# Performance work log

Hardware: AMD Instinct MI355X
Metric: run time of the kernel (lower is better)

The kernel has to match this reference:

```python
import jax, jax.numpy as jnp
import numpy as np

B, T, F, H, D, L = 64, 1024, 304, 304, 128, 128  # batch, enc len, feat=emb, hidden, dict_size, max_phn_num


def _init(k, sh):
    bound = 1.0 / np.sqrt(H)
    return jax.random.uniform(k, sh, jnp.float32, -bound, bound)


def setup_inputs() -> dict:
    key = jax.random.key(0)
    ks = jax.random.split(key, 12)
    return {
        "x": jax.random.normal(ks[0], (B, T, F), jnp.float32),
        "target": jax.random.randint(ks[1], (B, L, 1), 0, D),
        "emb": jax.random.normal(ks[2], (D, F), jnp.float32),
        "enc_Wih": _init(ks[3], (3 * H, F)),
        "enc_Whh": _init(ks[4], (3 * H, H)),
        "enc_bih": _init(ks[5], (3 * H,)),
        "enc_bhh": _init(ks[6], (3 * H,)),
        "dec_Wih": _init(ks[7], (3 * H, F)),
        "dec_Whh": _init(ks[8], (3 * H, H)),
        "dec_bih": _init(ks[9], (3 * H,)),
        "dec_bhh": _init(ks[10], (3 * H,)),
        "lin_W": _init(ks[11], (D, H)),
        "lin_b": jnp.zeros((D,), jnp.float32),
    }


def gru_step(h, xt, Wih, Whh, bih, bhh):
    # PyTorch GRU cell, gate order (r, z, n)
    gi = xt @ Wih.T + bih            # [B, 3H]
    gh = h @ Whh.T + bhh             # [B, 3H]
    ir, iz, innew = jnp.split(gi, 3, axis=-1)
    hr, hz, hn = jnp.split(gh, 3, axis=-1)
    r = jax.nn.sigmoid(ir + hr)
    z = jax.nn.sigmoid(iz + hz)
    n = jnp.tanh(innew + r * hn)
    return (1.0 - z) * n + z * h


def reference(x, target, emb, enc_Wih, enc_Whh, enc_bih, enc_bhh,
              dec_Wih, dec_Whh, dec_bih, dec_bhh, lin_W, lin_b):
    Bsz = x.shape[0]
    Hdim = enc_Whh.shape[1]
    Lphn = target.shape[1]

    # ---- encoder GRU over acoustic frames ----
    h0 = jnp.zeros((Bsz, Hdim), x.dtype)

    def enc_scan(h, xt):
        return gru_step(h, xt, enc_Wih, enc_Whh, enc_bih, enc_bhh), None

    h_enc, _ = jax.lax.scan(enc_scan, h0, jnp.swapaxes(x, 0, 1))

    tok0 = target[:, 0, 0]  # [B]

    def dec_scan(carry, _):
        h, tok = carry
        e = emb[tok]                                   # [B, F]
        h = gru_step(h, e, dec_Wih, dec_Whh, dec_bih, dec_bhh)
        logits = h @ lin_W.T + lin_b                   # [B, D]
        nxt = jnp.argmax(logits, axis=-1)
        return (h, nxt), logits

    _, logits = jax.lax.scan(dec_scan, (h_enc, tok0), None, length=Lphn)
    softmaxs = jnp.swapaxes(logits, 0, 1)              # [B, L, D]

    softmax_cal = softmaxs[:, :-1, :].reshape(-1, softmaxs.shape[-1])
    target_cal = target[:, 1:, :].reshape(-1)
    asr_outputs = jnp.argmax(softmaxs[:, :-1, :], axis=2)[:, :, None]
    return softmax_cal, target_cal, asr_outputs
```

## Files before the change

kernel.cpp:

```cpp
#include <hip/hip_runtime.h>
#include <cstdint>
#include <cstddef>

#define HN 304
#define G3 912
#define US 76
#define RS 228
#define NB 64
#define TSTEPS 1024
#define LDEC 127
#define DCLS 128

#define OUT_O1 1040384
#define OUT_O2 1048512

static const size_t OFF_GI   = 0;
static const size_t OFF_HP   = 239075328ull;
static const size_t OFF_AM   = 239230976ull;
static const size_t OFF_ABRT = 239233024ull;
static const size_t OFF_TAB  = 239233280ull;
static const size_t WS_NEED  = 239700224ull;

__global__ __launch_bounds__(256) void gi_gemm(const float* __restrict__ X,
                                               const float* __restrict__ W,
                                               const float* __restrict__ bias,
                                               float* __restrict__ out)
{
    __shared__ float As[16][132];
    __shared__ float Bs[16][132];
    const int tid = threadIdx.x;
    const int m0 = blockIdx.x * 128;
    const int n0 = blockIdx.y * 128;
    const int tx = tid & 15;
    const int ty = tid >> 4;
    const int lr = tid >> 1;
    const int lc = (tid & 1) * 8;

    float c[8][8];
#pragma unroll
    for (int i = 0; i < 8; ++i)
#pragma unroll
        for (int j = 0; j < 8; ++j) c[i][j] = 0.f;

    const bool wok = (n0 + lr < G3);
    const float* xrow = X + (size_t)(m0 + lr) * HN;
    const float* wrow = W + (size_t)(n0 + lr) * HN;
    const float4 z4 = make_float4(0.f, 0.f, 0.f, 0.f);

    float4 xa = *(const float4*)(xrow + lc);
    float4 xb = *(const float4*)(xrow + lc + 4);
    float4 wa = wok ? *(const float4*)(wrow + lc) : z4;
    float4 wb = wok ? *(const float4*)(wrow + lc + 4) : z4;

    for (int k0 = 0; k0 < HN; k0 += 16) {
        As[lc + 0][lr] = xa.x; As[lc + 1][lr] = xa.y; As[lc + 2][lr] = xa.z; As[lc + 3][lr] = xa.w;
        As[lc + 4][lr] = xb.x; As[lc + 5][lr] = xb.y; As[lc + 6][lr] = xb.z; As[lc + 7][lr] = xb.w;
        Bs[lc + 0][lr] = wa.x; Bs[lc + 1][lr] = wa.y; Bs[lc + 2][lr] = wa.z; Bs[lc + 3][lr] = wa.w;
        Bs[lc + 4][lr] = wb.x; Bs[lc + 5][lr] = wb.y; Bs[lc + 6][lr] = wb.z; Bs[lc + 7][lr] = wb.w;
        __syncthreads();
        if (k0 + 16 < HN) {
            xa = *(const float4*)(xrow + k0 + 16 + lc);
            xb = *(const float4*)(xrow + k0 + 16 + lc + 4);
            if (wok) {
                wa = *(const float4*)(wrow + k0 + 16 + lc);
                wb = *(const float4*)(wrow + k0 + 16 + lc + 4);
            }
        }
#pragma unroll
        for (int kk = 0; kk < 16; ++kk) {
            const float4 a0 = *(const float4*)&As[kk][ty * 8];
            const float4 a1 = *(const float4*)&As[kk][ty * 8 + 4];
            const float4 b0 = *(const float4*)&Bs[kk][tx * 8];
            const float4 b1 = *(const float4*)&Bs[kk][tx * 8 + 4];
            c[0][0] += a0.x * b0.x; c[0][1] += a0.x * b0.y; c[0][2] += a0.x * b0.z; c[0][3] += a0.x * b0.w;
            c[0][4] += a0.x * b1.x; c[0][5] += a0.x * b1.y; c[0][6] += a0.x * b1.z; c[0][7] += a0.x * b1.w;
            c[1][0] += a0.y * b0.x; c[1][1] += a0.y * b0.y; c[1][2] += a0.y * b0.z; c[1][3] += a0.y * b0.w;
            c[1][4] += a0.y * b1.x; c[1][5] += a0.y * b1.y; c[1][6] += a0.y * b1.z; c[1][7] += a0.y * b1.w;
            c[2][0] += a0.z * b0.x; c[2][1] += a0.z * b0.y; c[2][2] += a0.z * b0.z; c[2][3] += a0.z * b0.w;
            c[2][4] += a0.z * b1.x; c[2][5] += a0.z * b1.y; c[2][6] += a0.z * b1.z; c[2][7] += a0.z * b1.w;
            c[3][0] += a0.w * b0.x; c[3][1] += a0.w * b0.y; c[3][2] += a0.w * b0.z; c[3][3] += a0.w * b0.w;
            c[3][4] += a0.w * b1.x; c[3][5] += a0.w * b1.y; c[3][6] += a0.w * b1.z; c[3][7] += a0.w * b1.w;
            c[4][0] += a1.x * b0.x; c[4][1] += a1.x * b0.y; c[4][2] += a1.x * b0.z; c[4][3] += a1.x * b0.w;
            c[4][4] += a1.x * b1.x; c[4][5] += a1.x * b1.y; c[4][6] += a1.x * b1.z; c[4][7] += a1.x * b1.w;
            c[5][0] += a1.y * b0.x; c[5][1] += a1.y * b0.y; c[5][2] += a1.y * b0.z; c[5][3] += a1.y * b0.w;
            c[5][4] += a1.y * b1.x; c[5][5] += a1.y * b1.y; c[5][6] += a1.y * b1.z; c[5][7] += a1.y * b1.w;
            c[6][0] += a1.z * b0.x; c[6][1] += a1.z * b0.y; c[6][2] += a1.z * b0.z; c[6][3] += a1.z * b0.w;
            c[6][4] += a1.z * b1.x; c[6][5] += a1.z * b1.y; c[6][6] += a1.z * b1.z; c[6][7] += a1.z * b1.w;
            c[7][0] += a1.w * b0.x; c[7][1] += a1.w * b0.y; c[7][2] += a1.w * b0.z; c[7][3] += a1.w * b0.w;
            c[7][4] += a1.w * b1.x; c[7][5] += a1.w * b1.y; c[7][6] += a1.w * b1.z; c[7][7] += a1.w * b1.w;
        }
        __syncthreads();
    }

    const int nb = n0 + tx * 8;
    float4 bb0 = (nb + 3 < G3) ? *(const float4*)(bias + nb) : z4;
    float4 bb1 = (nb + 7 < G3) ? *(const float4*)(bias + nb + 4) : z4;
#pragma unroll
    for (int i = 0; i < 8; ++i) {
        const size_t m = (size_t)(m0 + ty * 8 + i);
        if (nb + 3 < G3) {
            float4 v = make_float4(c[i][0] + bb0.x, c[i][1] + bb0.y, c[i][2] + bb0.z, c[i][3] + bb0.w);
            *(float4*)(out + m * G3 + nb) = v;
        }
        if (nb + 7 < G3) {
            float4 v = make_float4(c[i][4] + bb1.x, c[i][5] + bb1.y, c[i][6] + bb1.z, c[i][7] + bb1.w);
            *(float4*)(out + m * G3 + nb + 4) = v;
        }
    }
}

__global__ __launch_bounds__(256) void table_k(const float* __restrict__ emb,
                                               const float* __restrict__ Wih,
                                               const float* __restrict__ bih,
                                               float* __restrict__ tab)
{
    const int idx = blockIdx.x * 256 + threadIdx.x;
    const int d = idx / G3;
    const int R = idx - d * G3;
    const float4* e4 = (const float4*)(emb + (size_t)d * HN);
    const float4* w4 = (const float4*)(Wih + (size_t)R * HN);
    float acc = 0.f;
#pragma unroll
    for (int j = 0; j < 76; ++j) {
        const float4 e = e4[j], w = w4[j];
        acc += e.x * w.x; acc += e.y * w.y; acc += e.z * w.z; acc += e.w * w.w;
    }
    tab[idx] = acc + bih[R];
}

__global__ void tcal_k(const int* __restrict__ target, float* __restrict__ out)
{
    const int i = blockIdx.x * 256 + threadIdx.x;
    if (i < NB * LDEC) {
        const int b = i / LDEC;
        const int t = i - b * LDEC;
        out[OUT_O1 + i] = (float)target[b * 128 + t + 1];
    }
}

__device__ __forceinline__ unsigned poll_tag32(unsigned int* p, unsigned want, int* abortf)
{
    unsigned v; int g = 0;
    for (;;) {
        v = __hip_atomic_load(p, __ATOMIC_RELAXED, __HIP_MEMORY_SCOPE_AGENT);
        if ((v & 3u) == want) break;
        if ((++g & 255) == 0) {
            if (__hip_atomic_load(abortf, __ATOMIC_RELAXED, __HIP_MEMORY_SCOPE_AGENT) != 0) break;
            if (g > (1 << 19)) {
                __hip_atomic_store(abortf, 1, __ATOMIC_RELAXED, __HIP_MEMORY_SCOPE_AGENT);
                break;
            }
        }
    }
    __asm__ volatile("" ::: "memory");
    return v;
}

__device__ __forceinline__ unsigned long long spin_tag(unsigned long long* p, int want, int* abortf)
{
    int g = 0;
    unsigned long long r;
    for (;;) {
        r = __hip_atomic_load(p, __ATOMIC_RELAXED, __HIP_MEMORY_SCOPE_AGENT);
        if ((int)(r >> 32) >= want) break;
        if ((++g & 255) == 0) {
            if (__hip_atomic_load(abortf, __ATOMIC_RELAXED, __HIP_MEMORY_SCOPE_AGENT) != 0) break;
            if (g > (1 << 19)) {
                __hip_atomic_store(abortf, 1, __ATOMIC_RELAXED, __HIP_MEMORY_SCOPE_AGENT);
                break;
            }
        }
    }
    __asm__ volatile("" ::: "memory");
    return r;
}

__global__ __launch_bounds__(512, 2) void rnn_persist(
    const float* __restrict__ gi,
    const float* __restrict__ encWhh, const float* __restrict__ encBhh,
    const float* __restrict__ decWhh, const float* __restrict__ decBhh,
    const float* __restrict__ tab,
    const float* __restrict__ linW, const float* __restrict__ linB,
    const int* __restrict__ target,
    unsigned int* hpk, unsigned long long* amax, int* abortf, float* out)
{
    const int w = blockIdx.x;
    const int b = w & 63;
    const int s = w >> 6;
    const int tid = threadIdx.x;

    __shared__ alignas(16) float hbuf[HN];
    __shared__ alignas(16) float part[4][RS];
    __shared__ alignas(16) float lpart[32][9];
    __shared__ float logit_s[32];
    __shared__ float amx_v[4];
    __shared__ int   amx_i[4];

    const bool comp = (tid < 456);
    const int ksq = tid / 114;
    const int lp  = tid - ksq * 114;
    const int g0 = lp / US,        ul0 = lp - g0 * US;
    const int g1 = (lp + 114) / US, ul1 = (lp + 114) - g1 * US;
    const int Rrow0 = g0 * HN + s * US + ul0;
    const int Rrow1 = g1 * HN + s * US + ul1;
    const int u = s * US + tid;
    const int cq = tid / US;

    unsigned long long* amx = amax + b * 4;
    unsigned int* hpb = hpk + b * HN;

    float4 wreg0[19], wreg1[19];
    if (comp) {
        const float4* wp0 = (const float4*)(encWhh + (size_t)Rrow0 * HN + (size_t)ksq * US);
        const float4* wp1 = (const float4*)(encWhh + (size_t)Rrow1 * HN + (size_t)ksq * US);
#pragma unroll
        for (int j = 0; j < 19; ++j) { wreg0[j] = wp0[j]; wreg1[j] = wp1[j]; }
    }
    float b_r = 0.f, b_z = 0.f, b_n = 0.f;
    if (tid < US) { b_r = encBhh[u]; b_z = encBhh[HN + u]; b_n = encBhh[2 * HN + u]; }

    for (int i = tid; i < HN; i += 512) hbuf[i] = 0.f;
    __syncthreads();

    const float* gib = gi + (size_t)b * TSTEPS * G3;

    for (int t = 0; t < TSTEPS; ++t) {
        const int T = t + 1;
        float gr = 0.f, gz = 0.f, gn = 0.f;
        if (tid < US) {
            const float* gp = gib + (size_t)t * G3;
            gr = gp[u]; gz = gp[HN + u]; gn = gp[2 * HN + u];
        }
        if (comp) {
            const float4* hp = (const float4*)(hbuf + ksq * US);
            float acc0 = 0.f, acc1 = 0.f;
#pragma unroll
            for (int j = 0; j < 19; ++j) {
                const float4 h4 = hp[j];
                const float4 w0 = wreg0[j], w1 = wreg1[j];
                acc0 += w0.x * h4.x; acc0 += w0.y * h4.y; acc0 += w0.z * h4.z; acc0 += w0.w * h4.w;
                acc1 += w1.x * h4.x; acc1 += w1.y * h4.y; acc1 += w1.z * h4.z; acc1 += w1.w * h4.w;
            }
            part[ksq][lp] = acc0;
            part[ksq][lp + 114] = acc1;
        }
        __syncthreads();
        if (tid < US) {
            const float ghr = part[0][tid] + part[1][tid] + part[2][tid] + part[3][tid] + b_r;
            const float ghz = part[0][US + tid] + part[1][US + tid] + part[2][US + tid] + part[3][US + tid] + b_z;
            const float ghn = part[0][2 * US + tid] + part[1][2 * US + tid] + part[2][2 * US + tid] + part[3][2 * US + tid] + b_n;
            const float r = 1.f / (1.f + expf(-(gr + ghr)));
            const float z = 1.f / (1.f + expf(-(gz + ghz)));
            const float n = tanhf(gn + r * ghn);
            const float hnew = (1.f - z) * n + z * hbuf[u];
            const unsigned hb = (__float_as_uint(hnew) & ~3u) | ((unsigned)T & 3u);
            hbuf[u] = __uint_as_float(hb);
            __hip_atomic_store(&hpb[(T & 1) * NB * HN + u], hb,
                               __ATOMIC_RELAXED, __HIP_MEMORY_SCOPE_AGENT);
        }
        if (tid < HN && cq != s) {
            const unsigned v = poll_tag32(&hpb[(T & 1) * NB * HN + tid],
                                          (unsigned)T & 3u, abortf);
            hbuf[tid] = __uint_as_float(v);
        }
        __syncthreads();
    }

    if (comp) {
        const float4* wp0 = (const float4*)(decWhh + (size_t)Rrow0 * HN + (size_t)ksq * US);
        const float4* wp1 = (const float4*)(decWhh + (size_t)Rrow1 * HN + (size_t)ksq * US);
#pragma unroll
        for (int j = 0; j < 19; ++j) { wreg0[j] = wp0[j]; wreg1[j] = wp1[j]; }
    }
    if (tid < US) { b_r = decBhh[u]; b_z = decBhh[HN + u]; b_n = decBhh[2 * HN + u]; }
    int tok = target[b * 128];
    const int lrow = tid >> 3;
    const int lks = tid & 7;
    __syncthreads();

    for (int t = 0; t < LDEC; ++t) {
        const int T = TSTEPS + 1 + t;
        float gr = 0.f, gz = 0.f, gn = 0.f;
        if (tid < US) {
            const float* tp = tab + (size_t)tok * G3;
            gr = tp[u]; gz = tp[HN + u]; gn = tp[2 * HN + u];
        }
        if (comp) {
            const float4* hp = (const float4*)(hbuf + ksq * US);
            float acc0 = 0.f, acc1 = 0.f;
#pragma unroll
            for (int j = 0; j < 19; ++j) {
                const float4 h4 = hp[j];
                const float4 w0 = wreg0[j], w1 = wreg1[j];
                acc0 += w0.x * h4.x; acc0 += w0.y * h4.y; acc0 += w0.z * h4.z; acc0 += w0.w * h4.w;
                acc1 += w1.x * h4.x; acc1 += w1.y * h4.y; acc1 += w1.z * h4.z; acc1 += w1.w * h4.w;
            }
            part[ksq][lp] = acc0;
            part[ksq][lp + 114] = acc1;
        }
        __syncthreads();
        if (tid < US) {
            const float ghr = part[0][tid] + part[1][tid] + part[2][tid] + part[3][tid] + b_r;
            const float ghz = part[0][US + tid] + part[1][US + tid] + part[2][US + tid] + part[3][US + tid] + b_z;
            const float ghn = part[0][2 * US + tid] + part[1][2 * US + tid] + part[2][2 * US + tid] + part[3][2 * US + tid] + b_n;
            const float r = 1.f / (1.f + expf(-(gr + ghr)));
            const float z = 1.f / (1.f + expf(-(gz + ghz)));
            const float n = tanhf(gn + r * ghn);
            const float hnew = (1.f - z) * n + z * hbuf[u];
            const unsigned hb = (__float_as_uint(hnew) & ~3u) | ((unsigned)T & 3u);
            hbuf[u] = __uint_as_float(hb);
            __hip_atomic_store(&hpb[(T & 1) * NB * HN + u], hb,
                               __ATOMIC_RELAXED, __HIP_MEMORY_SCOPE_AGENT);
        }
        if (tid < HN && cq != s) {
            const unsigned v = poll_tag32(&hpb[(T & 1) * NB * HN + tid],
                                          (unsigned)T & 3u, abortf);
            hbuf[tid] = __uint_as_float(v);
        }
        __syncthreads();

        if (tid < 256) {
            const float2* wl = (const float2*)(linW + (size_t)(s * 32 + lrow) * HN + (size_t)lks * 38);
            const float2* hl = (const float2*)(hbuf + lks * 38);
            float a = 0.f;
#pragma unroll
            for (int j = 0; j < 19; ++j) { const float2 wv = wl[j], hv = hl[j]; a += wv.x * hv.x; a += wv.y * hv.y; }
            lpart[lrow][lks] = a;
        }
        __syncthreads();
        if (tid < 32) {
            const float lg = lpart[tid][0] + lpart[tid][1] + lpart[tid][2] + lpart[tid][3]
                           + lpart[tid][4] + lpart[tid][5] + lpart[tid][6] + lpart[tid][7]
                           + linB[s * 32 + tid];
            logit_s[tid] = lg;
            out[((size_t)b * LDEC + t) * DCLS + s * 32 + tid] = lg;
        }
        __syncthreads();
        if (tid == 0) {
            float bv = logit_s[0]; int bi = 0;
            for (int i = 1; i < 32; ++i) { const float v = logit_s[i]; if (v > bv) { bv = v; bi = i; } }
            const unsigned tagf = (unsigned)(((t + 1) << 8) | (s * 32 + bi));
            const unsigned long long pk = ((unsigned long long)tagf << 32) | (unsigned long long)__float_as_uint(bv);
            __hip_atomic_store(&amx[s], pk, __ATOMIC_RELAXED, __HIP_MEMORY_SCOPE_AGENT);
        }
        if (tid < 4) {
            const unsigned long long r = spin_tag(&amx[tid], (t + 1) << 8, abortf);
            amx_v[tid] = __uint_as_float((unsigned)r);
            amx_i[tid] = (int)(r >> 32) & 255;
        }
        __syncthreads();
        {
            float gbv = amx_v[0]; int gbi = amx_i[0];
            if (amx_v[1] > gbv) { gbv = amx_v[1]; gbi = amx_i[1]; }
            if (amx_v[2] > gbv) { gbv = amx_v[2]; gbi = amx_i[2]; }
            if (amx_v[3] > gbv) { gbv = amx_v[3]; gbi = amx_i[3]; }
            tok = gbi;
            if (tid == 0 && s == 0) out[OUT_O2 + (size_t)b * LDEC + t] = (float)gbi;
        }
    }
}

extern "C" void kernel_launch(void* const* d_in, const int* in_sizes, int n_in,
                              void* d_out, int out_size, void* d_ws, size_t ws_size,
                              hipStream_t stream)
{
    (void)in_sizes; (void)n_in; (void)out_size;
    const float* x      = (const float*)d_in[0];
    const int*   target = (const int*)  d_in[1];
    const float* emb    = (const float*)d_in[2];
    const float* encWih = (const float*)d_in[3];
    const float* encWhh = (const float*)d_in[4];
    const float* encBih = (const float*)d_in[5];
    const float* encBhh = (const float*)d_in[6];
    const float* decWih = (const float*)d_in[7];
    const float* decWhh = (const float*)d_in[8];
    const float* decBih = (const float*)d_in[9];
    const float* decBhh = (const float*)d_in[10];
    const float* linW   = (const float*)d_in[11];
    const float* linB   = (const float*)d_in[12];
    float* out = (float*)d_out;
    char* ws = (char*)d_ws;

    if (ws_size < WS_NEED) return;

    float*              gi   = (float*)(ws + OFF_GI);
    unsigned int*       hpk  = (unsigned int*)(ws + OFF_HP);
    unsigned long long* amax = (unsigned long long*)(ws + OFF_AM);
    int*                abrt = (int*)(ws + OFF_ABRT);
    float*              tab  = (float*)(ws + OFF_TAB);

    hipMemsetAsync(ws + OFF_HP, 0, OFF_TAB - OFF_HP, stream);
    gi_gemm<<<dim3(512, 8), 256, 0, stream>>>(x, encWih, encBih, gi);
    table_k<<<456, 256, 0, stream>>>(emb, decWih, decBih, tab);
    tcal_k<<<32, 256, 0, stream>>>(target, out);
    rnn_persist<<<256, 512, 0, stream>>>(gi, encWhh, encBhh, decWhh, decBhh, tab,
                                         linW, linB, target, hpk, amax, abrt, out);
}
```

Before: 3.064 ms.

## Compute full logits redundantly per block to drop cross-block argmax exchange

Each of the four blocks per batch row now stages all of lin_W in shared memory, computes all 128 logits itself and takes a local argmax, which removes the per-step global atomic publish/spin on the amax slots. The encoder loop is also unrolled by two so the next step's gate inputs are loaded ahead, and __syncthreads is replaced by a lighter lgkmcnt+s_barrier. The cost is about 160KB of dynamic shared memory per block, which may limit residency, plus four times the logit work.

Result: slower. 3.179 ms (+3.8%).

```diff
diff --git a/kernel.cpp b/kernel.cpp
--- a/kernel.cpp
+++ b/kernel.cpp
@@ -20,6 +20,14 @@
 static const size_t OFF_ABRT = 239233024ull;
 static const size_t OFF_TAB  = 239233280ull;
 static const size_t WS_NEED  = 239700224ull;
+
+#define SM_LINW   0
+#define SM_U      39040
+#define SM_HB     40192
+#define SM_AMXV   40496
+#define SM_AMXI   40500
+#define SM_FLOATS 40512
+#define SMEM_BYTES (SM_FLOATS * 4)
 
 __global__ __launch_bounds__(256) void gi_gemm(const float* __restrict__ X,
                                                const float* __restrict__ W,
@@ -138,6 +146,16 @@
     }
 }
 
+__device__ __forceinline__ void barl()
+{
+    asm volatile("s_waitcnt lgkmcnt(0)\n\ts_barrier" ::: "memory");
+}
+
+__device__ __forceinline__ void pub32(unsigned int* p, unsigned v)
+{
+    __hip_atomic_store(p, v, __ATOMIC_RELAXED, __HIP_MEMORY_SCOPE_AGENT);
+}
+
 __device__ __forceinline__ unsigned poll_tag32(unsigned int* p, unsigned want, int* abortf)
 {
     unsigned v; int g = 0;
@@ -156,24 +174,45 @@
     return v;
 }
 
-__device__ __forceinline__ unsigned long long spin_tag(unsigned long long* p, int want, int* abortf)
-{
-    int g = 0;
-    unsigned long long r;
-    for (;;) {
-        r = __hip_atomic_load(p, __ATOMIC_RELAXED, __HIP_MEMORY_SCOPE_AGENT);
-        if ((int)(r >> 32) >= want) break;
-        if ((++g & 255) == 0) {
-            if (__hip_atomic_load(abortf, __ATOMIC_RELAXED, __HIP_MEMORY_SCOPE_AGENT) != 0) break;
-            if (g > (1 << 19)) {
-                __hip_atomic_store(abortf, 1, __ATOMIC_RELAXED, __HIP_MEMORY_SCOPE_AGENT);
-                break;
-            }
-        }
-    }
-    __asm__ volatile("" ::: "memory");
-    return r;
-}
+#define RNN_STEP(T_, GR, GZ, GN) do {                                               \
+    if (comp) {                                                                     \
+        const float4* hp = (const float4*)(hbuf + ksq * US);                        \
+        float acc0 = 0.f, acc1 = 0.f;                                               \
+        _Pragma("unroll")                                                           \
+        for (int j = 0; j < 19; ++j) {                                              \
+            const float4 h4 = hp[j];                                                \
+            const float4 w0 = wreg0[j], w1 = wreg1[j];                              \
+            acc0 += w0.x * h4.x; acc0 += w0.y * h4.y;                               \
+            acc0 += w0.z * h4.z; acc0 += w0.w * h4.w;                               \
+            acc1 += w1.x * h4.x; acc1 += w1.y * h4.y;                               \
+            acc1 += w1.z * h4.z; acc1 += w1.w * h4.w;                               \
+        }                                                                           \
+        partU[ksq * RS + lp] = acc0;                                                \
+        partU[ksq * RS + lp + 114] = acc1;                                          \
+    }                                                                               \
+    barl();                                                                         \
+    if (tid < US) {                                                                 \
+        const float ghr = partU[tid] + partU[RS + tid]                              \
+                        + partU[2 * RS + tid] + partU[3 * RS + tid] + b_r;          \
+        const float ghz = partU[US + tid] + partU[RS + US + tid]                    \
+                        + partU[2 * RS + US + tid] + partU[3 * RS + US + tid] + b_z;\
+        const float ghn = partU[2 * US + tid] + partU[RS + 2 * US + tid]            \
+                        + partU[2 * RS + 2 * US + tid] + partU[3 * RS + 2 * US + tid] + b_n; \
+        const float r_ = 1.f / (1.f + expf(-((GR) + ghr)));                         \
+        const float z_ = 1.f / (1.f + expf(-((GZ) + ghz)));                         \
+        const float n_ = tanhf((GN) + r_ * ghn);                                    \
+        const float hnew = (1.f - z_) * n_ + z_ * hbuf[u];                          \
+        const unsigned hb_ = (__float_as_uint(hnew) & ~3u) | ((unsigned)(T_) & 3u); \
+        hbuf[u] = __uint_as_float(hb_);                                             \
+        pub32(&hpb[((T_) & 1) * NB * HN + u], hb_);                                 \
+    }                                                                               \
+    if (tid < HN && cq != s) {                                                      \
+        const unsigned v_ = poll_tag32(&hpb[((T_) & 1) * NB * HN + tid],            \
+                                       (unsigned)(T_) & 3u, abortf);                \
+        hbuf[tid] = __uint_as_float(v_);                                            \
+    }                                                                               \
+    barl();                                                                         \
+} while (0)
 
 __global__ __launch_bounds__(512, 2) void rnn_persist(
     const float* __restrict__ gi,
@@ -182,32 +221,37 @@
     const float* __restrict__ tab,
     const float* __restrict__ linW, const float* __restrict__ linB,
     const int* __restrict__ target,
-    unsigned int* hpk, unsigned long long* amax, int* abortf, float* out)
+    unsigned int* hpk, int* abortf, float* out)
 {
     const int w = blockIdx.x;
     const int b = w & 63;
     const int s = w >> 6;
     const int tid = threadIdx.x;
 
-    __shared__ alignas(16) float hbuf[HN];
-    __shared__ alignas(16) float part[4][RS];
-    __shared__ alignas(16) float lpart[32][9];
-    __shared__ float logit_s[32];
-    __shared__ float amx_v[4];
-    __shared__ int   amx_i[4];
+    extern __shared__ float smem[];
+    float* linw_s = smem + SM_LINW;
+    float* partU  = smem + SM_U;
+    float* hbuf   = smem + SM_HB;
+    float* amx_vs = smem + SM_AMXV;
+    int*   amx_is = (int*)(smem + SM_AMXI);
 
     const bool comp = (tid < 456);
     const int ksq = tid / 114;
     const int lp  = tid - ksq * 114;
-    const int g0 = lp / US,        ul0 = lp - g0 * US;
+    const int g0 = lp / US,         ul0 = lp - g0 * US;
     const int g1 = (lp + 114) / US, ul1 = (lp + 114) - g1 * US;
     const int Rrow0 = g0 * HN + s * US + ul0;
     const int Rrow1 = g1 * HN + s * US + ul1;
     const int u = s * US + tid;
     const int cq = tid / US;
 
-    unsigned long long* amx = amax + b * 4;
     unsigned int* hpb = hpk + b * HN;
+
+    for (int i = tid; i < DCLS * HN; i += 512) {
+        const int r0 = i / HN;
+        linw_s[r0 * 305 + (i - r0 * HN)] = linW[i];
+    }
+    for (int i = tid; i < HN; i += 512) hbuf[i] = 0.f;
 
     float4 wreg0[19], wreg1[19];
     if (comp) {
@@ -219,51 +263,24 @@
     float b_r = 0.f, b_z = 0.f, b_n = 0.f;
     if (tid < US) { b_r = encBhh[u]; b_z = encBhh[HN + u]; b_n = encBhh[2 * HN + u]; }
 
-    for (int i = tid; i < HN; i += 512) hbuf[i] = 0.f;
     __syncthreads();
 
     const float* gib = gi + (size_t)b * TSTEPS * G3;
 
-    for (int t = 0; t < TSTEPS; ++t) {
-        const int T = t + 1;
-        float gr = 0.f, gz = 0.f, gn = 0.f;
+    float grA = 0.f, gzA = 0.f, gnA = 0.f, grB = 0.f, gzB = 0.f, gnB = 0.f;
+    if (tid < US) { grA = gib[u]; gzA = gib[HN + u]; gnA = gib[2 * HN + u]; }
+
+    for (int t = 0; t < TSTEPS; t += 2) {
         if (tid < US) {
-            const float* gp = gib + (size_t)t * G3;
-            gr = gp[u]; gz = gp[HN + u]; gn = gp[2 * HN + u];
-        }
-        if (comp) {
-            const float4* hp = (const float4*)(hbuf + ksq * US);
-            float acc0 = 0.f, acc1 = 0.f;
-#pragma unroll
-            for (int j = 0; j < 19; ++j) {
-                const float4 h4 = hp[j];
-                const float4 w0 = wreg0[j], w1 = wreg1[j];
-                acc0 += w0.x * h4.x; acc0 += w0.y * h4.y; acc0 += w0.z * h4.z; acc0 += w0.w * h4.w;
-                acc1 += w1.x * h4.x; acc1 += w1.y * h4.y; acc1 += w1.z * h4.z; acc1 += w1.w * h4.w;
-            }
-            part[ksq][lp] = acc0;
-            part[ksq][lp + 114] = acc1;
-        }
-        __syncthreads();
-        if (tid < US) {
-            const float ghr = part[0][tid] + part[1][tid] + part[2][tid] + part[3][tid] + b_r;
-            const float ghz = part[0][US + tid] + part[1][US + tid] + part[2][US + tid] + part[3][US + tid] + b_z;
-            const float ghn = part[0][2 * US + tid] + part[1][2 * US + tid] + part[2][2 * US + tid] + part[3][2 * US + tid] + b_n;
-            const float r = 1.f / (1.f + expf(-(gr + ghr)));
-            const float z = 1.f / (1.f + expf(-(gz + ghz)));
-            const float n = tanhf(gn + r * ghn);
-            const float hnew = (1.f - z) * n + z * hbuf[u];
-            const unsigned hb = (__float_as_uint(hnew) & ~3u) | ((unsigned)T & 3u);
-            hbuf[u] = __uint_as_float(hb);
-            __hip_atomic_store(&hpb[(T & 1) * NB * HN + u], hb,
-                               __ATOMIC_RELAXED, __HIP_MEMORY_SCOPE_AGENT);
-        }
-        if (tid < HN && cq != s) {
-            const unsigned v = poll_tag32(&hpb[(T & 1) * NB * HN + tid],
-                                          (unsigned)T & 3u, abortf);
-            hbuf[tid] = __uint_as_float(v);
-        }
-        __syncthreads();
+            const float* gp = gib + (size_t)(t + 1) * G3;
+            grB = gp[u]; gzB = gp[HN + u]; gnB = gp[2 * HN + u];
+        }
+        RNN_STEP(t + 1, grA, gzA, gnA);
+        if (tid < US && t + 2 < TSTEPS) {
+            const float* gp = gib + (size_t)(t + 2) * G3;
+            grA = gp[u]; gzA = gp[HN + u]; gnA = gp[2 * HN + u];
+        }
+        RNN_STEP(t + 2, grB, gzB, gnB);
     }
 
     if (comp) {
@@ -274,9 +291,11 @@
     }
     if (tid < US) { b_r = decBhh[u]; b_z = decBhh[HN + u]; b_n = decBhh[2 * HN + u]; }
     int tok = target[b * 128];
-    const int lrow = tid >> 3;
-    const int lks = tid & 7;
-    __syncthreads();
+    float linb_r = 0.f;
+    if (tid < DCLS) linb_r = linB[tid];
+    const int lr128 = tid & 127;
+    const int lq = tid >> 7;
+    barl();
 
     for (int t = 0; t < LDEC; ++t) {
         const int T = TSTEPS + 1 + t;
@@ -285,75 +304,50 @@
             const float* tp = tab + (size_t)tok * G3;
             gr = tp[u]; gz = tp[HN + u]; gn = tp[2 * HN + u];
         }
-        if (comp) {
-            const float4* hp = (const float4*)(hbuf + ksq * US);
-            float acc0 = 0.f, acc1 = 0.f;
+        RNN_STEP(T, gr, gz, gn);
+
+        {
+            const float* wl = linw_s + lr128 * 305 + lq * 76;
+            const float* hl = hbuf + lq * 76;
+            float a0 = 0.f, a1 = 0.f;
 #pragma unroll
             for (int j = 0; j < 19; ++j) {
-                const float4 h4 = hp[j];
-                const float4 w0 = wreg0[j], w1 = wreg1[j];
-                acc0 += w0.x * h4.x; acc0 += w0.y * h4.y; acc0 += w0.z * h4.z; acc0 += w0.w * h4.w;
-                acc1 += w1.x * h4.x; acc1 += w1.y * h4.y; acc1 += w1.z * h4.z; acc1 += w1.w * h4.w;
-            }
-            part[ksq][lp] = acc0;
-            part[ksq][lp + 114] = acc1;
-        }
-        __syncthreads();
-        if (tid < US) {
-            const float ghr = part[0][tid] + part[1][tid] + part[2][tid] + part[3][tid] + b_r;
-            const float ghz = part[0][US + tid] + part[1][US + tid] + part[2][US + tid] + part[3][US + tid] + b_z;
-            const float ghn = part[0][2 * US + tid] + part[1][2 * US + tid] + part[2][2 * US + tid] + part[3][2 * US + tid] + b_n;
-            const float r = 1.f / (1.f + expf(-(gr + ghr)));
-            const float z = 1.f / (1.f + expf(-(gz + ghz)));
-            const float n = tanhf(gn + r * ghn);
-            const float hnew = (1.f - z) * n + z * hbuf[u];
-            const unsigned hb = (__float_as_uint(hnew) & ~3u) | ((unsigned)T & 3u);
-            hbuf[u] = __uint_as_float(hb);
-            __hip_atomic_store(&hpb[(T & 1) * NB * HN + u], hb,
-                               __ATOMIC_RELAXED, __HIP_MEMORY_SCOPE_AGENT);
-        }
-        if (tid < HN && cq != s) {
-            const unsigned v = poll_tag32(&hpb[(T & 1) * NB * HN + tid],
-                                          (unsigned)T & 3u, abortf);
-            hbuf[tid] = __uint_as_float(v);
-        }
-        __syncthreads();
-
-        if (tid < 256) {
-            const float2* wl = (const float2*)(linW + (size_t)(s * 32 + lrow) * HN + (size_t)lks * 38);
-            const float2* hl = (const float2*)(hbuf + lks * 38);
-            float a = 0.f;
-#pragma unroll
-            for (int j = 0; j < 19; ++j) { const float2 wv = wl[j], hv = hl[j]; a += wv.x * hv.x; a += wv.y * hv.y; }
-            lpart[lrow][lks] = a;
-        }
-        __syncthreads();
-        if (tid < 32) {
-            const float lg = lpart[tid][0] + lpart[tid][1] + lpart[tid][2] + lpart[tid][3]
-                           + lpart[tid][4] + lpart[tid][5] + lpart[tid][6] + lpart[tid][7]
-                           + linB[s * 32 + tid];
-            logit_s[tid] = lg;
-            out[((size_t)b * LDEC + t) * DCLS + s * 32 + tid] = lg;
-        }
-        __syncthreads();
-        if (tid == 0) {
-            float bv = logit_s[0]; int bi = 0;
-            for (int i = 1; i < 32; ++i) { const float v = logit_s[i]; if (v > bv) { bv = v; bi = i; } }
-            const unsigned tagf = (unsigned)(((t + 1) << 8) | (s * 32 + bi));
-            const unsigned long long pk = ((unsigned long long)tagf << 32) | (unsigned long long)__float_as_uint(bv);
-            __hip_atomic_store(&amx[s], pk, __ATOMIC_RELAXED, __HIP_MEMORY_SCOPE_AGENT);
-        }
+                a0 += wl[2 * j] * hl[2 * j];
+                a0 += wl[2 * j + 1] * hl[2 * j + 1];
+            }
+#pragma unroll
+            for (int j = 0; j < 19; ++j) {
+                a1 += wl[38 + 2 * j] * hl[38 + 2 * j];
+                a1 += wl[38 + 2 * j + 1] * hl[38 + 2 * j + 1];
+            }
+            partU[lr128 * 9 + 2 * lq]     = a0;
+            partU[lr128 * 9 + 2 * lq + 1] = a1;
+        }
+        barl();
+        if (tid < DCLS) {
+            float lg = partU[tid * 9 + 0];
+            lg += partU[tid * 9 + 1]; lg += partU[tid * 9 + 2]; lg += partU[tid * 9 + 3];
+            lg += partU[tid * 9 + 4]; lg += partU[tid * 9 + 5]; lg += partU[tid * 9 + 6];
+            lg += partU[tid * 9 + 7]; lg += linb_r;
+            if ((tid >> 5) == s)
+                out[((size_t)b * LDEC + t) * DCLS + tid] = lg;
+            partU[tid * 9 + 8] = lg;
+        }
+        barl();
         if (tid < 4) {
-            const unsigned long long r = spin_tag(&amx[tid], (t + 1) << 8, abortf);
-            amx_v[tid] = __uint_as_float((unsigned)r);
-            amx_i[tid] = (int)(r >> 32) & 255;
-        }
-        __syncthreads();
+            float bv = partU[(tid * 32) * 9 + 8]; int bi = 0;
+            for (int i = 1; i < 32; ++i) {
+                const float v = partU[(tid * 32 + i) * 9 + 8];
+                if (v > bv) { bv = v; bi = i; }
+            }
+            amx_vs[tid] = bv; amx_is[tid] = tid * 32 + bi;
+        }
+        barl();
         {
-            float gbv = amx_v[0]; int gbi = amx_i[0];
-            if (amx_v[1] > gbv) { gbv = amx_v[1]; gbi = amx_i[1]; }
-            if (amx_v[2] > gbv) { gbv = amx_v[2]; gbi = amx_i[2]; }
-            if (amx_v[3] > gbv) { gbv = amx_v[3]; gbi = amx_i[3]; }
+            float gbv = amx_vs[0]; int gbi = amx_is[0];
+            if (amx_vs[1] > gbv) { gbv = amx_vs[1]; gbi = amx_is[1]; }
+            if (amx_vs[2] > gbv) { gbv = amx_vs[2]; gbi = amx_is[2]; }
+            if (amx_vs[3] > gbv) { gbv = amx_vs[3]; gbi = amx_is[3]; }
             tok = gbi;
             if (tid == 0 && s == 0) out[OUT_O2 + (size_t)b * LDEC + t] = (float)gbi;
         }
@@ -383,16 +377,22 @@
 
     if (ws_size < WS_NEED) return;
 
-    float*              gi   = (float*)(ws + OFF_GI);
-    unsigned int*       hpk  = (unsigned int*)(ws + OFF_HP);
-    unsigned long long* amax = (unsigned long long*)(ws + OFF_AM);
-    int*                abrt = (int*)(ws + OFF_ABRT);
-    float*              tab  = (float*)(ws + OFF_TAB);
+    float*        gi   = (float*)(ws + OFF_GI);
+    unsigned int* hpk  = (unsigned int*)(ws + OFF_HP);
+    int*          abrt = (int*)(ws + OFF_ABRT);
+    float*        tab  = (float*)(ws + OFF_TAB);
+
+    static bool s_attr_done = false;
+    if (!s_attr_done) {
+        hipFuncSetAttribute(reinterpret_cast<const void*>(rnn_persist),
+                            hipFuncAttributeMaxDynamicSharedMemorySize, SMEM_BYTES);
+        s_attr_done = true;
+    }
 
     hipMemsetAsync(ws + OFF_HP, 0, OFF_TAB - OFF_HP, stream);
     gi_gemm<<<dim3(512, 8), 256, 0, stream>>>(x, encWih, encBih, gi);
     table_k<<<456, 256, 0, stream>>>(emb, decWih, decBih, tab);
     tcal_k<<<32, 256, 0, stream>>>(target, out);
-    rnn_persist<<<256, 512, 0, stream>>>(gi, encWhh, encBhh, decWhh, decBhh, tab,
-                                         linW, linB, target, hpk, amax, abrt, out);
-}
+    rnn_persist<<<256, 512, SMEM_BYTES, stream>>>(gi, encWhh, encBhh, decWhh, decBhh, tab,
+                                                  linW, linB, target, hpk, abrt, out);
+}
```

## Stage half of recurrent weights in LDS and use packed FMA in input GEMM

Applied to the files above, without the earlier changes.

The persistent RNN kernel now keeps only one of its two recurrent-weight row slices in registers. The second slice is staged into about 145KB of dynamic shared memory in an interleaved layout, which removes register pressure and possible spills at the cost of an LDS read each step. The input-projection GEMM switches to inline v_pk_fma_f32 with float2 accumulators to double FMA throughput per instruction. The large dynamic LDS allocation limits the kernel to one block per CU, which may matter for the 256-block persistent launch.

Result: slower. 3.339 ms (+9.0%).

```diff
diff --git a/kernel.cpp b/kernel.cpp
--- a/kernel.cpp
+++ b/kernel.cpp
@@ -20,6 +20,23 @@
 static const size_t OFF_ABRT = 239233024ull;
 static const size_t OFF_TAB  = 239233280ull;
 static const size_t WS_NEED  = 239700224ull;
+
+#define SM_W2T    0
+#define SM_HB     34656
+#define SM_PART   34960
+#define SM_LPART  35872
+#define SM_LOGS   36160
+#define SM_AMXV   36192
+#define SM_AMXI   36196
+#define SM_FLOATS 36200
+#define SMEM_BYTES (SM_FLOATS * 4)
+
+#define PKFMA_L(C2, A2, B2) \
+    asm("v_pk_fma_f32 %0, %1, %2, %0 op_sel:[0,0,0] op_sel_hi:[0,1,1]" \
+        : "+v"(C2) : "v"(A2), "v"(B2))
+#define PKFMA_H(C2, A2, B2) \
+    asm("v_pk_fma_f32 %0, %1, %2, %0 op_sel:[1,0,0] op_sel_hi:[1,1,1]" \
+        : "+v"(C2) : "v"(A2), "v"(B2))
 
 __global__ __launch_bounds__(256) void gi_gemm(const float* __restrict__ X,
                                                const float* __restrict__ W,
@@ -36,11 +53,11 @@
     const int lr = tid >> 1;
     const int lc = (tid & 1) * 8;
 
-    float c[8][8];
+    float2 c2[8][4];
 #pragma unroll
     for (int i = 0; i < 8; ++i)
 #pragma unroll
-        for (int j = 0; j < 8; ++j) c[i][j] = 0.f;
+        for (int j = 0; j < 4; ++j) { c2[i][j].x = 0.f; c2[i][j].y = 0.f; }
 
     const bool wok = (n0 + lr < G3);
     const float* xrow = X + (size_t)(m0 + lr) * HN;
@@ -68,26 +85,19 @@
         }
 #pragma unroll
         for (int kk = 0; kk < 16; ++kk) {
-            const float4 a0 = *(const float4*)&As[kk][ty * 8];
-            const float4 a1 = *(const float4*)&As[kk][ty * 8 + 4];
-            const float4 b0 = *(const float4*)&Bs[kk][tx * 8];
-            const float4 b1 = *(const float4*)&Bs[kk][tx * 8 + 4];
-            c[0][0] += a0.x * b0.x; c[0][1] += a0.x * b0.y; c[0][2] += a0.x * b0.z; c[0][3] += a0.x * b0.w;
-            c[0][4] += a0.x * b1.x; c[0][5] += a0.x * b1.y; c[0][6] += a0.x * b1.z; c[0][7] += a0.x * b1.w;
-            c[1][0] += a0.y * b0.x; c[1][1] += a0.y * b0.y; c[1][2] += a0.y * b0.z; c[1][3] += a0.y * b0.w;
-            c[1][4] += a0.y * b1.x; c[1][5] += a0.y * b1.y; c[1][6] += a0.y * b1.z; c[1][7] += a0.y * b1.w;
-            c[2][0] += a0.z * b0.x; c[2][1] += a0.z * b0.y; c[2][2] += a0.z * b0.z; c[2][3] += a0.z * b0.w;
-            c[2][4] += a0.z * b1.x; c[2][5] += a0.z * b1.y; c[2][6] += a0.z * b1.z; c[2][7] += a0.z * b1.w;
-            c[3][0] += a0.w * b0.x; c[3][1] += a0.w * b0.y; c[3][2] += a0.w * b0.z; c[3][3] += a0.w * b0.w;
-            c[3][4] += a0.w * b1.x; c[3][5] += a0.w * b1.y; c[3][6] += a0.w * b1.z; c[3][7] += a0.w * b1.w;
-            c[4][0] += a1.x * b0.x; c[4][1] += a1.x * b0.y; c[4][2] += a1.x * b0.z; c[4][3] += a1.x * b0.w;
-            c[4][4] += a1.x * b1.x; c[4][5] += a1.x * b1.y; c[4][6] += a1.x * b1.z; c[4][7] += a1.x * b1.w;
-            c[5][0] += a1.y * b0.x; c[5][1] += a1.y * b0.y; c[5][2] += a1.y * b0.z; c[5][3] += a1.y * b0.w;
-            c[5][4] += a1.y * b1.x; c[5][5] += a1.y * b1.y; c[5][6] += a1.y * b1.z; c[5][7] += a1.y * b1.w;
-            c[6][0] += a1.z * b0.x; c[6][1] += a1.z * b0.y; c[6][2] += a1.z * b0.z; c[6][3] += a1.z * b0.w;
-            c[6][4] += a1.z * b1.x; c[6][5] += a1.z * b1.y; c[6][6] += a1.z * b1.z; c[6][7] += a1.z * b1.w;
-            c[7][0] += a1.w * b0.x; c[7][1] += a1.w * b0.y; c[7][2] += a1.w * b0.z; c[7][3] += a1.w * b0.w;
-            c[7][4] += a1.w * b1.x; c[7][5] += a1.w * b1.y; c[7][6] += a1.w * b1.z; c[7][7] += a1.w * b1.w;
+            const float2* ar = (const float2*)&As[kk][ty * 8];
+            const float2* br = (const float2*)&Bs[kk][tx * 8];
+            float2 ap[4], bp[4];
+#pragma unroll
+            for (int j = 0; j < 4; ++j) { ap[j] = ar[j]; bp[j] = br[j]; }
+#pragma unroll
+            for (int p = 0; p < 4; ++p) {
+#pragma unroll
+                for (int j = 0; j < 4; ++j) {
+                    PKFMA_L(c2[2 * p][j],     ap[p], bp[j]);
+                    PKFMA_H(c2[2 * p + 1][j], ap[p], bp[j]);
+                }
+            }
         }
         __syncthreads();
     }
@@ -99,11 +109,13 @@
     for (int i = 0; i < 8; ++i) {
         const size_t m = (size_t)(m0 + ty * 8 + i);
         if (nb + 3 < G3) {
-            float4 v = make_float4(c[i][0] + bb0.x, c[i][1] + bb0.y, c[i][2] + bb0.z, c[i][3] + bb0.w);
+            float4 v = make_float4(c2[i][0].x + bb0.x, c2[i][0].y + bb0.y,
+                                   c2[i][1].x + bb0.z, c2[i][1].y + bb0.w);
             *(float4*)(out + m * G3 + nb) = v;
         }
         if (nb + 7 < G3) {
-            float4 v = make_float4(c[i][4] + bb1.x, c[i][5] + bb1.y, c[i][6] + bb1.z, c[i][7] + bb1.w);
+            float4 v = make_float4(c2[i][2].x + bb1.x, c2[i][2].y + bb1.y,
+                                   c2[i][3].x + bb1.z, c2[i][3].y + bb1.w);
             *(float4*)(out + m * G3 + nb + 4) = v;
         }
     }
@@ -189,37 +201,54 @@
     const int s = w >> 6;
     const int tid = threadIdx.x;
 
-    __shared__ alignas(16) float hbuf[HN];
-    __shared__ alignas(16) float part[4][RS];
-    __shared__ alignas(16) float lpart[32][9];
-    __shared__ float logit_s[32];
-    __shared__ float amx_v[4];
-    __shared__ int   amx_i[4];
+    extern __shared__ float smem[];
+    float* w2t     = smem + SM_W2T;
+    float* hbuf    = smem + SM_HB;
+    float* partU   = smem + SM_PART;
+    float* lpartU  = smem + SM_LPART;
+    float* logit_s = smem + SM_LOGS;
+    float* amx_v   = smem + SM_AMXV;
+    int*   amx_i   = (int*)(smem + SM_AMXI);
 
     const bool comp = (tid < 456);
     const int ksq = tid / 114;
     const int lp  = tid - ksq * 114;
     const int g0 = lp / US,        ul0 = lp - g0 * US;
-    const int g1 = (lp + 114) / US, ul1 = (lp + 114) - g1 * US;
     const int Rrow0 = g0 * HN + s * US + ul0;
-    const int Rrow1 = g1 * HN + s * US + ul1;
     const int u = s * US + tid;
     const int cq = tid / US;
 
     unsigned long long* amx = amax + b * 4;
     unsigned int* hpb = hpk + b * HN;
 
-    float4 wreg0[19], wreg1[19];
+    auto stage_w2 = [&](const float* __restrict__ W) {
+        for (int i = tid; i < 34656; i += 512) {
+            const int e   = i & 3;
+            const int blk = i >> 2;
+            const int lp_ = blk % 114;
+            const int kj  = blk / 114;
+            const int j_  = kj % 19;
+            const int kq_ = kj / 19;
+            const int l2  = lp_ + 114;
+            const int g1_ = l2 / US;
+            const int ul_ = l2 - g1_ * US;
+            const int row = g1_ * HN + s * US + ul_;
+            w2t[i] = W[(size_t)row * HN + kq_ * US + j_ * 4 + e];
+        }
+    };
+    stage_w2(encWhh);
+
+    for (int i = tid; i < HN; i += 512) hbuf[i] = 0.f;
+
+    float4 wreg0[19];
     if (comp) {
         const float4* wp0 = (const float4*)(encWhh + (size_t)Rrow0 * HN + (size_t)ksq * US);
-        const float4* wp1 = (const float4*)(encWhh + (size_t)Rrow1 * HN + (size_t)ksq * US);
-#pragma unroll
-        for (int j = 0; j < 19; ++j) { wreg0[j] = wp0[j]; wreg1[j] = wp1[j]; }
+#pragma unroll
+        for (int j = 0; j < 19; ++j) wreg0[j] = wp0[j];
     }
     float b_r = 0.f, b_z = 0.f, b_n = 0.f;
     if (tid < US) { b_r = encBhh[u]; b_z = encBhh[HN + u]; b_n = encBhh[2 * HN + u]; }
 
-    for (int i = tid; i < HN; i += 512) hbuf[i] = 0.f;
     __syncthreads();
 
     const float* gib = gi + (size_t)b * TSTEPS * G3;
@@ -233,22 +262,24 @@
         }
         if (comp) {
             const float4* hp = (const float4*)(hbuf + ksq * US);
+            const float4* wb = (const float4*)w2t + (ksq * 19) * 114 + lp;
             float acc0 = 0.f, acc1 = 0.f;
 #pragma unroll
             for (int j = 0; j < 19; ++j) {
                 const float4 h4 = hp[j];
-                const float4 w0 = wreg0[j], w1 = wreg1[j];
+                const float4 w0 = wreg0[j];
+                const float4 w1 = wb[j * 114];
                 acc0 += w0.x * h4.x; acc0 += w0.y * h4.y; acc0 += w0.z * h4.z; acc0 += w0.w * h4.w;
                 acc1 += w1.x * h4.x; acc1 += w1.y * h4.y; acc1 += w1.z * h4.z; acc1 += w1.w * h4.w;
             }
-            part[ksq][lp] = acc0;
-            part[ksq][lp + 114] = acc1;
+            partU[ksq * RS + lp] = acc0;
+            partU[ksq * RS + lp + 114] = acc1;
         }
         __syncthreads();
         if (tid < US) {
-            const float ghr = part[0][tid] + part[1][tid] + part[2][tid] + part[3][tid] + b_r;
-            const float ghz = part[0][US + tid] + part[1][US + tid] + part[2][US + tid] + part[3][US + tid] + b_z;
-            const float ghn = part[0][2 * US + tid] + part[1][2 * US + tid] + part[2][2 * US + tid] + part[3][2 * US + tid] + b_n;
+            const float ghr = partU[tid] + partU[RS + tid] + partU[2 * RS + tid] + partU[3 * RS + tid] + b_r;
+            const float ghz = partU[US + tid] + partU[RS + US + tid] + partU[2 * RS + US + tid] + partU[3 * RS + US + tid] + b_z;
+            const float ghn = partU[2 * US + tid] + partU[RS + 2 * US + tid] + partU[2 * RS + 2 * US + tid] + partU[3 * RS + 2 * US + tid] + b_n;
             const float r = 1.f / (1.f + expf(-(gr + ghr)));
             const float z = 1.f / (1.f + expf(-(gz + ghz)));
             const float n = tanhf(gn + r * ghn);
@@ -266,11 +297,11 @@
         __syncthreads();
     }
 
+    stage_w2(decWhh);
     if (comp) {
         const float4* wp0 = (const float4*)(decWhh + (size_t)Rrow0 * HN + (size_t)ksq * US);
-        const float4* wp1 = (const float4*)(decWhh + (size_t)Rrow1 * HN + (size_t)ksq * US);
-#pragma unroll
-        for (int j = 0; j < 19; ++j) { wreg0[j] = wp0[j]; wreg1[j] = wp1[j]; }
+#pragma unroll
+        for (int j = 0; j < 19; ++j) wreg0[j] = wp0[j];
     }
     if (tid < US) { b_r = decBhh[u]; b_z = decBhh[HN + u]; b_n = decBhh[2 * HN + u]; }
     int tok = target[b * 128];
@@ -287,22 +318,24 @@
         }
         if (comp) {
             const float4* hp = (const float4*)(hbuf + ksq * US);
+            const float4* wb = (const float4*)w2t + (ksq * 19) * 114 + lp;
             float acc0 = 0.f, acc1 = 0.f;
 #pragma unroll
             for (int j = 0; j < 19; ++j) {
                 const float4 h4 = hp[j];
-                const float4 w0 = wreg0[j], w1 = wreg1[j];
+                const float4 w0 = wreg0[j];
+                const float4 w1 = wb[j * 114];
                 acc0 += w0.x * h4.x; acc0 += w0.y * h4.y; acc0 += w0.z * h4.z; acc0 += w0.w * h4.w;
                 acc1 += w1.x * h4.x; acc1 += w1.y * h4.y; acc1 += w1.z * h4.z; acc1 += w1.w * h4.w;
             }
-            part[ksq][lp] = acc0;
-            part[ksq][lp + 114] = acc1;
+            partU[ksq * RS + lp] = acc0;
+            partU[ksq * RS + lp + 114] = acc1;
         }
         __syncthreads();
         if (tid < US) {
-            const float ghr = part[0][tid] + part[1][tid] + part[2][tid] + part[3][tid] + b_r;
-            const float ghz = part[0][US + tid] + part[1][US + tid] + part[2][US + tid] + part[3][US + tid] + b_z;
-            const float ghn = part[0][2 * US + tid] + part[1][2 * US + tid] + part[2][2 * US + tid] + part[3][2 * US + tid] + b_n;
+            const float ghr = partU[tid] + partU[RS + tid] + partU[2 * RS + tid] + partU[3 * RS + tid] + b_r;
+            const float ghz = partU[US + tid] + partU[RS + US + tid] + partU[2 * RS + US + tid] + partU[3 * RS + US + tid] + b_z;
+            const float ghn = partU[2 * US + tid] + partU[RS + 2 * US + tid] + partU[2 * RS + 2 * US + tid] + partU[3 * RS + 2 * US + tid] + b_n;
             const float r = 1.f / (1.f + expf(-(gr + ghr)));
             const float z = 1.f / (1.f + expf(-(gz + ghz)));
             const float n = tanhf(gn + r * ghn);
@@ -325,12 +358,12 @@
             float a = 0.f;
 #pragma unroll
             for (int j = 0; j < 19; ++j) { const float2 wv = wl[j], hv = hl[j]; a += wv.x * hv.x; a += wv.y * hv.y; }
-            lpart[lrow][lks] = a;
+            lpartU[lrow * 9 + lks] = a;
         }
         __syncthreads();
         if (tid < 32) {
-            const float lg = lpart[tid][0] + lpart[tid][1] + lpart[tid][2] + lpart[tid][3]
-                           + lpart[tid][4] + lpart[tid][5] + lpart[tid][6] + lpart[tid][7]
+            const float lg = lpartU[tid * 9 + 0] + lpartU[tid * 9 + 1] + lpartU[tid * 9 + 2] + lpartU[tid * 9 + 3]
+                           + lpartU[tid * 9 + 4] + lpartU[tid * 9 + 5] + lpartU[tid * 9 + 6] + lpartU[tid * 9 + 7]
                            + linB[s * 32 + tid];
             logit_s[tid] = lg;
             out[((size_t)b * LDEC + t) * DCLS + s * 32 + tid] = lg;
@@ -389,10 +422,17 @@
     int*                abrt = (int*)(ws + OFF_ABRT);
     float*              tab  = (float*)(ws + OFF_TAB);
 
-    hipMemsetAsync(ws + OFF_HP, 0, OFF_TAB - OFF_HP, stream);
+    static bool s_attr_done = false;
+    if (!s_attr_done) {
+        (void)hipFuncSetAttribute(reinterpret_cast<const void*>(rnn_persist),
+                                  hipFuncAttributeMaxDynamicSharedMemorySize, SMEM_BYTES);
+        s_attr_done = true;
+    }
+
+    (void)hipMemsetAsync(ws + OFF_HP, 0, OFF_TAB - OFF_HP, stream);
     gi_gemm<<<dim3(512, 8), 256, 0, stream>>>(x, encWih, encBih, gi);
     table_k<<<456, 256, 0, stream>>>(emb, decWih, decBih, tab);
     tcal_k<<<32, 256, 0, stream>>>(target, out);
-    rnn_persist<<<256, 512, 0, stream>>>(gi, encWhh, encBhh, decWhh, decBhh, tab,
-                                         linW, linB, target, hpk, amax, abrt, out);
-}
+    rnn_persist<<<256, 512, SMEM_BYTES, stream>>>(gi, encWhh, encBhh, decWhh, decBhh, tab,
+                                                  linW, linB, target, hpk, amax, abrt, out);
+}
```
